# Performance work log

Measured on AMD Instinct MI355X. Metric: run time of the kernel, lower is better.

Reference implementation:

```python
import jax, jax.numpy as jnp
import numpy as np

N_PAIRS = 64000
N_ATOMS = 16000
N_PAIR_FEATURES = 8
N_HIDDEN = 100


def setup_inputs() -> dict:
    key = jax.random.key(0)
    k1, k2, k3, k4 = jax.random.split(key, 4)
    pair_features = jax.random.normal(k1, (N_PAIRS, N_PAIR_FEATURES), dtype=jnp.float32)
    atom_features = jax.random.normal(k2, (N_ATOMS, N_HIDDEN), dtype=jnp.float32)
    atom_to_pair = jax.random.randint(k3, (N_PAIRS, 2), 0, N_ATOMS, dtype=jnp.int32)
    W = jax.random.normal(k4, (N_PAIR_FEATURES, N_HIDDEN * N_HIDDEN), dtype=jnp.float32) * 0.1
    b = jnp.zeros((N_HIDDEN * N_HIDDEN,), dtype=jnp.float32)
    return {"pair_features": pair_features, "atom_features": atom_features,
            "atom_to_pair": atom_to_pair, "W": W, "b": b}


def reference(pair_features, atom_features, atom_to_pair, W, b):
    n_atoms, n_hidden = atom_features.shape
    # Dense projection: [E, F] @ [F, H*H] -> per-edge HxH matrices
    A = (pair_features @ W + b).reshape(-1, n_hidden, n_hidden)  # [E, H, H]
    # Gather source-atom features (column 1 of atom_to_pair)
    src = atom_features[atom_to_pair[:, 1]]                      # [E, H]
    # Batched matrix-vector multiply per edge
    msg = jnp.einsum('eij,ej->ei', A, src)                       # [E, H]
    # Scatter-reduce messages onto destination atoms (column 0)
    return jax.ops.segment_sum(msg, atom_to_pair[:, 0], num_segments=n_atoms)
```

## Files before the change

kernel.cpp:

```cpp
#include <hip/hip_runtime.h>
#include <hip/hip_bf16.h>

#define N_PAIRS   64000
#define N_ATOMS   16000
#define N_FEAT    8
#define N_HIDDEN  100
#define SW        1024
#define SKL       936
#define MAX_DEG   64

#define AFB_BLOCKS   1563
#define SETUP_BLOCKS (112 * 1024 / 256)
#define HIST_BLOCKS  (N_PAIRS / 256)

typedef __attribute__((ext_vector_type(8))) short bf16x8_t;
typedef __attribute__((ext_vector_type(4))) float f32x4_t;

__global__ __launch_bounds__(256) void setup_hist(const float* __restrict__ W,
                                                  const float* __restrict__ b,
                                                  const int* __restrict__ a2p,
                                                  const float* __restrict__ af,
                                                  __hip_bfloat16* __restrict__ wtb2,
                                                  unsigned short* __restrict__ afb,
                                                  int* __restrict__ deg,
                                                  unsigned* __restrict__ bucket) {
    int bid = blockIdx.x;
    if (bid < AFB_BLOCKS) {
        int id = bid * 256 + threadIdx.x;
        if (id < 400000) {
            float4 v = ((const float4*)af)[id];
            ushort4 h;
            h.x = (unsigned short)(__float_as_uint(v.x) >> 16);
            h.y = (unsigned short)(__float_as_uint(v.y) >> 16);
            h.z = (unsigned short)(__float_as_uint(v.z) >> 16);
            h.w = (unsigned short)(__float_as_uint(v.w) >> 16);
            ((ushort4*)afb)[id] = h;
        }
    } else if (bid < AFB_BLOCKS + SETUP_BLOCKS) {
        int id = (bid - AFB_BLOCKS) * 256 + threadIdx.x;
        int i = id >> 10;
        int k = id & 1023;
        float v = 0.f;
        if (i < N_HIDDEN) {
            if (k < 800) {
                int f = k / N_HIDDEN;
                int j = k - f * N_HIDDEN;
                v = W[f * (N_HIDDEN * N_HIDDEN) + i * N_HIDDEN + j];
            } else if (k < 900) {
                int j = k - 800;
                v = b[i * N_HIDDEN + j];
            }
        }
        wtb2[id] = __float2bfloat16(v);
    } else {
        int e = (bid - AFB_BLOCKS - SETUP_BLOCKS) * 256 + threadIdx.x;
        int dest = a2p[e * 2];
        int src  = a2p[e * 2 + 1];
        int slot = atomicAdd(&deg[dest], 1);
        if (slot < MAX_DEG)
            bucket[dest * MAX_DEG + slot] = ((unsigned)e << 14) | (unsigned)src;
    }
}

__global__ __launch_bounds__(512) void fused_edge_gemm(const unsigned short* __restrict__ afb,
                                                       const float* __restrict__ pf,
                                                       const int* __restrict__ deg,
                                                       const unsigned* __restrict__ bucket,
                                                       const __hip_bfloat16* __restrict__ wtb2,
                                                       float* __restrict__ out) {
    __shared__ __hip_bfloat16 St[16 * SKL];
    int blk  = blockIdx.x;
    int wave = threadIdx.x >> 6;
    int lane = threadIdx.x & 63;
    bool act = (lane < 50);

#pragma unroll
    for (int j = 0; j < 2; ++j) {
        int r = wave * 2 + j;
        int d = __builtin_amdgcn_readfirstlane(blk * 16 + r);
        int n = deg[d];
        if (n > 32) n = 32;

        const unsigned* sb = bucket + (size_t)d * MAX_DEG;

        float acc[9][2] = {};
        for (int t0 = 0; t0 < n; t0 += 4) {
            unsigned pk[4];
#pragma unroll
            for (int u = 0; u < 4; ++u)
                pk[u] = sb[(t0 + u) < n ? (t0 + u) : 0];
            float2 a[4];
#pragma unroll
            for (int u = 0; u < 4; ++u) {
                int src = (int)(pk[u] & 16383u);
                if ((t0 + u) < n && act) {
                    unsigned uu = *(const unsigned*)(afb + src * N_HIDDEN + 2 * lane);
                    a[u].x = __uint_as_float(uu << 16);
                    a[u].y = __uint_as_float(uu & 0xffff0000u);
                } else {
                    a[u] = make_float2(0.f, 0.f);
                }
            }
#pragma unroll
            for (int u = 0; u < 4; ++u) {
                int e = (int)(pk[u] >> 14);
                const float* pe = pf + e * N_FEAT;
#pragma unroll
                for (int f = 0; f < N_FEAT; ++f) {
                    float p = pe[f];
                    acc[f][0] += p * a[u].x;
                    acc[f][1] += p * a[u].y;
                }
                acc[8][0] += a[u].x;
                acc[8][1] += a[u].y;
            }
        }

        __hip_bfloat16* srow = St + r * SKL;
        if (act) {
#pragma unroll
            for (int f = 0; f < 9; ++f) {
                __hip_bfloat162 h;
                h.x = __float2bfloat16(acc[f][0]);
                h.y = __float2bfloat16(acc[f][1]);
                *(__hip_bfloat162*)(srow + f * N_HIDDEN + 2 * lane) = h;
            }
        } else {
            __hip_bfloat162 z;
            z.x = __float2bfloat16(0.f);
            z.y = z.x;
            *(__hip_bfloat162*)(srow + 900 + 2 * (lane - 50)) = z;
        }
    }
    __syncthreads();

    if (wave < 7) {
        int quad = lane >> 4;
        int l15  = lane & 15;
        int m0   = blk * 16;
        const __hip_bfloat16* as = St + l15 * SKL + quad * 8;
        const __hip_bfloat16* bp = wtb2 + (size_t)(wave * 16 + l15) * SW + quad * 8;
        f32x4_t accd = {0.f, 0.f, 0.f, 0.f};
#pragma unroll
        for (int k = 0; k < 29; ++k) {
            bf16x8_t aa = *(const bf16x8_t*)(as + k * 32);
            bf16x8_t bb = *(const bf16x8_t*)(bp + k * 32);
            accd = __builtin_amdgcn_mfma_f32_16x16x32_bf16(aa, bb, accd, 0, 0, 0);
        }
        int c = wave * 16 + l15;
        if (c < N_HIDDEN) {
#pragma unroll
            for (int rr = 0; rr < 4; ++rr)
                out[(size_t)(m0 + quad * 4 + rr) * N_HIDDEN + c] = accd[rr];
        }
    }
}

extern "C" void kernel_launch(void* const* d_in, const int* in_sizes, int n_in,
                              void* d_out, int out_size, void* d_ws, size_t ws_size,
                              hipStream_t stream) {
    const float* pf  = (const float*)d_in[0];
    const float* af  = (const float*)d_in[1];
    const int*   a2p = (const int*)d_in[2];
    const float* W   = (const float*)d_in[3];
    const float* b   = (const float*)d_in[4];
    float* out = (float*)d_out;

    char* ws = (char*)d_ws;
    __hip_bfloat16* wtb2 = (__hip_bfloat16*)ws;
    int* deg             = (int*)(ws + 229376);
    unsigned* bucket     = (unsigned*)(ws + 229376 + 64000);
    unsigned short* afb  = (unsigned short*)(ws + 229376 + 64000 + 4096000);

    hipMemsetAsync(deg, 0, N_ATOMS * sizeof(int), stream);
    setup_hist<<<AFB_BLOCKS + SETUP_BLOCKS + HIST_BLOCKS, 256, 0, stream>>>(
        W, b, a2p, af, wtb2, afb, deg, bucket);
    fused_edge_gemm<<<N_ATOMS / 16, 512, 0, stream>>>(afb, pf, deg, bucket, wtb2, out);
}
```

Measured before the change: 106.9 us.

## Prefetch first eight neighbor feature rows per atom into shared memory

Each wave loads the bucket entries for its two destination atoms up front. It then gathers the first eight source-atom bf16 feature rows per atom cooperatively into LDS, using 8-byte loads with half a wave per atom, before a block barrier. The accumulation loop reads these rows from LDS and falls back to the original global gather for neighbors beyond eight. The goal is more memory-level parallelism and fewer dependent gather latencies, at the cost of an extra barrier, more LDS use (lower occupancy), and a clamp on the edge index for padded slots.

```diff
diff --git a/kernel.cpp b/kernel.cpp
--- a/kernel.cpp
+++ b/kernel.cpp
@@ -7,6 +7,7 @@
 #define N_HIDDEN  100
 #define SW        1024
 #define SKL       936
+#define AST       104
 #define MAX_DEG   64
 
 #define AFB_BLOCKS   1563
@@ -69,22 +70,80 @@
                                                        const __hip_bfloat16* __restrict__ wtb2,
                                                        float* __restrict__ out) {
     __shared__ __hip_bfloat16 St[16 * SKL];
+    __shared__ __hip_bfloat16 Ast[16 * 8 * AST];
     int blk  = blockIdx.x;
     int wave = threadIdx.x >> 6;
     int lane = threadIdx.x & 63;
     bool act = (lane < 50);
 
+    int d0 = __builtin_amdgcn_readfirstlane(blk * 16 + 2 * wave);
+    int n0 = deg[d0];     if (n0 > 32) n0 = 32;
+    int n1 = deg[d0 + 1]; if (n1 > 32) n1 = 32;
+
+    const unsigned* sb0 = bucket + (size_t)d0 * MAX_DEG;
+    const unsigned* sb1 = sb0 + MAX_DEG;
+
+    unsigned pk0[8], pk1[8];
+#pragma unroll
+    for (int t = 0; t < 8; ++t) pk0[t] = sb0[t < n0 ? t : 0];
+#pragma unroll
+    for (int t = 0; t < 8; ++t) pk1[t] = sb1[t < n1 ? t : 0];
+
+    {
+        int h  = lane >> 5;
+        int l  = lane & 31;
+        int rg = wave * 2 + h;
+        int nh = h ? n1 : n0;
+        int nsh = nh < 8 ? nh : 8;
+        uint2 g[8];
+#pragma unroll
+        for (int t = 0; t < 8; ++t) {
+            unsigned pk = h ? pk1[t] : pk0[t];
+            int src = (int)(pk & 16383u);
+            if (t < nsh && l < 25)
+                g[t] = *(const uint2*)(afb + src * N_HIDDEN + 4 * l);
+            else
+                g[t] = make_uint2(0u, 0u);
+        }
+#pragma unroll
+        for (int t = 0; t < 8; ++t)
+            if (l < 25)
+                *(uint2*)(&Ast[(rg * 8 + t) * AST + 4 * l]) = g[t];
+    }
+    __syncthreads();
+
 #pragma unroll
     for (int j = 0; j < 2; ++j) {
         int r = wave * 2 + j;
-        int d = __builtin_amdgcn_readfirstlane(blk * 16 + r);
-        int n = deg[d];
-        if (n > 32) n = 32;
-
-        const unsigned* sb = bucket + (size_t)d * MAX_DEG;
+        int n = j ? n1 : n0;
+        int ns = n < 8 ? n : 8;
+        const unsigned* sb = j ? sb1 : sb0;
 
         float acc[9][2] = {};
-        for (int t0 = 0; t0 < n; t0 += 4) {
+#pragma unroll
+        for (int t = 0; t < 8; ++t) {
+            float2 a;
+            if (t < ns && act) {
+                unsigned uu = *(const unsigned*)(&Ast[(r * 8 + t) * AST + 2 * lane]);
+                a.x = __uint_as_float(uu << 16);
+                a.y = __uint_as_float(uu & 0xffff0000u);
+            } else {
+                a = make_float2(0.f, 0.f);
+            }
+            unsigned pk = j ? pk1[t] : pk0[t];
+            int e = (int)(pk >> 14);
+            if (e > 63999) e = 63999;
+            const float* pe = pf + e * N_FEAT;
+#pragma unroll
+            for (int f = 0; f < N_FEAT; ++f) {
+                float p = pe[f];
+                acc[f][0] += p * a.x;
+                acc[f][1] += p * a.y;
+            }
+            acc[8][0] += a.x;
+            acc[8][1] += a.y;
+        }
+        for (int t0 = 8; t0 < n; t0 += 4) {
             unsigned pk[4];
 #pragma unroll
             for (int u = 0; u < 4; ++u)
```

After: 113.6 us. +6.3%, slower.
